# Performance work log

Measured on AMD Instinct MI355X. Metric: run time of the kernel, lower is better.

## Reference

```python
import jax, jax.numpy as jnp
import numpy as np

TIME = 100.0   # self.time in the original module
TAU = 100.0    # decay constant: exp((t - time)/100)


def setup_inputs() -> dict:
    key = jax.random.key(0)
    k1, k2, k3, k4 = jax.random.split(key, 4)
    N, D, B, K = 500000, 128, 50000, 32
    nodes = jax.random.randint(k1, (B,), 0, N)
    neigh_ids = jax.random.randint(k2, (B, K), 0, N)
    # neighbor event times in [0, 200]; only t <= TIME are valid temporal neighbors
    neigh_times = jax.random.uniform(k3, (B, K), dtype=jnp.float32) * 200.0
    features = jax.random.normal(k4, (N, D), dtype=jnp.float32)
    return {"nodes": nodes, "neigh_ids": neigh_ids,
            "neigh_times": neigh_times, "features": features}


def reference(nodes, neigh_ids, neigh_times, features):
    # Time-decayed edge weights; neighbors with t > TIME are masked out
    # (equivalent to the searchsorted cutoff in the original code).
    w = jnp.where(neigh_times <= TIME, jnp.exp((neigh_times - TIME) / TAU), 0.0)  # [B,K]
    total = w.sum(-1)                               # total_value[i]
    total = jnp.where(total == 0.0, 1.0, total)     # fallback to 1 when no valid neighbor
    w = w / total[:, None]                          # dic_edge[i][j] / total_value[i]
    # self-loop weight 1, then row-normalize: num_neigh = 1 + sum_j w_ij
    denom = 1.0 + w.sum(-1)                         # [B]
    neigh_feats = jnp.einsum('bk,bkd->bd', w, features[neigh_ids])  # weighted neighbor sum
    out = (features[nodes] + neigh_feats) / denom[:, None]          # [B,D]
    return out
```

## Files before the change

### kernel.cpp

```cpp
#include <hip/hip_runtime.h>
#include <math.h>


__global__ __launch_bounds__(256) void mean_agg_kernel(
    const int*   __restrict__ nodes,
    const int*   __restrict__ neigh_ids,
    const float* __restrict__ neigh_times,
    const float* __restrict__ features,
    float*       __restrict__ out,
    int B)
{
    const int wave = threadIdx.x >> 6;
    const int lane = threadIdx.x & 63;
    const int row  = blockIdx.x * 4 + wave;
    if (row >= B) return;

    const int j = lane & 31;
    const float t  = neigh_times[row * 32 + j];
    const int  idj = neigh_ids[row * 32 + j];
    float wj = (t <= 100.0f) ? __expf((t - 100.0f) * 0.01f) : 0.0f;

    float S = wj;
    #pragma unroll
    for (int m = 1; m < 32; m <<= 1)
        S += __shfl_xor(S, m);

    const float T     = (S == 0.0f) ? 1.0f : S;
    const float denom = 1.0f + S / T;

    float2 acc = make_float2(0.0f, 0.0f);
    #pragma unroll 4
    for (int k = 0; k < 32; ++k) {
        const float wk = __shfl(wj, k);
        if (wk != 0.0f) {
            const int idk = __shfl(idj, k);
            const float2 f = *reinterpret_cast<const float2*>(
                &features[(size_t)idk * 128 + lane * 2]);
            acc.x += wk * f.x;
            acc.y += wk * f.y;
        }
    }

    const int self = nodes[row];
    const float2 fs = *reinterpret_cast<const float2*>(
        &features[(size_t)self * 128 + lane * 2]);

    const float inv_d  = 1.0f / denom;
    const float inv_td = 1.0f / (T * denom);
    float2 o;
    o.x = fs.x * inv_d + acc.x * inv_td;
    o.y = fs.y * inv_d + acc.y * inv_td;
    *reinterpret_cast<float2*>(&out[(size_t)row * 128 + lane * 2]) = o;
}

extern "C" void kernel_launch(void* const* d_in, const int* in_sizes, int n_in,
                              void* d_out, int out_size, void* d_ws, size_t ws_size,
                              hipStream_t stream) {
    const int*   nodes       = (const int*)  d_in[0];
    const int*   neigh_ids   = (const int*)  d_in[1];
    const float* neigh_times = (const float*)d_in[2];
    const float* features    = (const float*)d_in[3];
    float*       out         = (float*)      d_out;

    const int B = in_sizes[0];
    const int rows_per_block = 4;
    const int grid = (B + rows_per_block - 1) / rows_per_block;

    mean_agg_kernel<<<grid, 256, 0, stream>>>(nodes, neigh_ids, neigh_times,
                                              features, out, B);
}
```

Baseline: 78.60 us.

## Split wave into two half-waves gathering alternate neighbors with float4 loads

Each 64-lane wave now splits into two 32-lane halves. Each half gathers every other neighbor row using 16-byte float4 loads, so two neighbor rows are fetched per iteration, and the two partial sums are combined with a cross-half shuffle. Only the lower half writes the output. The goal is more memory-level parallelism and half as many dependent gather iterations. The cost is extra shuffles, a fully unrolled loop, and redundant self-feature loads in the upper half.

```diff
diff --git a/kernel.cpp b/kernel.cpp
--- a/kernel.cpp
+++ b/kernel.cpp
@@ -12,12 +12,13 @@
 {
     const int wave = threadIdx.x >> 6;
     const int lane = threadIdx.x & 63;
+    const int half = lane >> 5;
+    const int c    = lane & 31;
     const int row  = blockIdx.x * 4 + wave;
     if (row >= B) return;
 
-    const int j = lane & 31;
-    const float t  = neigh_times[row * 32 + j];
-    const int  idj = neigh_ids[row * 32 + j];
+    const float t  = neigh_times[row * 32 + c];
+    const int  idj = neigh_ids[row * 32 + c];
     float wj = (t <= 100.0f) ? __expf((t - 100.0f) * 0.01f) : 0.0f;
 
     float S = wj;
@@ -28,29 +29,40 @@
     const float T     = (S == 0.0f) ? 1.0f : S;
     const float denom = 1.0f + S / T;
 
-    float2 acc = make_float2(0.0f, 0.0f);
-    #pragma unroll 4
-    for (int k = 0; k < 32; ++k) {
-        const float wk = __shfl(wj, k);
+    float4 acc = make_float4(0.0f, 0.0f, 0.0f, 0.0f);
+    #pragma unroll
+    for (int i = 0; i < 16; ++i) {
+        const int   k   = 2 * i + half;
+        const float wk  = __shfl(wj, k);
+        const int   idk = __shfl(idj, k);
         if (wk != 0.0f) {
-            const int idk = __shfl(idj, k);
-            const float2 f = *reinterpret_cast<const float2*>(
-                &features[(size_t)idk * 128 + lane * 2]);
+            const float4 f = *reinterpret_cast<const float4*>(
+                &features[(size_t)idk * 128 + c * 4]);
             acc.x += wk * f.x;
             acc.y += wk * f.y;
+            acc.z += wk * f.z;
+            acc.w += wk * f.w;
         }
     }
+    acc.x += __shfl_xor(acc.x, 32);
+    acc.y += __shfl_xor(acc.y, 32);
+    acc.z += __shfl_xor(acc.z, 32);
+    acc.w += __shfl_xor(acc.w, 32);
 
     const int self = nodes[row];
-    const float2 fs = *reinterpret_cast<const float2*>(
-        &features[(size_t)self * 128 + lane * 2]);
+    const float4 fs = *reinterpret_cast<const float4*>(
+        &features[(size_t)self * 128 + c * 4]);
 
     const float inv_d  = 1.0f / denom;
     const float inv_td = 1.0f / (T * denom);
-    float2 o;
+    float4 o;
     o.x = fs.x * inv_d + acc.x * inv_td;
     o.y = fs.y * inv_d + acc.y * inv_td;
-    *reinterpret_cast<float2*>(&out[(size_t)row * 128 + lane * 2]) = o;
+    o.z = fs.z * inv_d + acc.z * inv_td;
+    o.w = fs.w * inv_d + acc.w * inv_td;
+
+    if (half == 0)
+        *reinterpret_cast<float4*>(&out[(size_t)row * 128 + c * 4]) = o;
 }
 
 extern "C" void kernel_launch(void* const* d_in, const int* in_sizes, int n_in,
```

Measured after the change: 72.41 us. 1.09x faster.

## Split wave into four neighbor groups with 32-byte loads and cross-lane reduction

Applied to the files above, without the earlier changes.

Each wave now processes four neighbors at once. Each 16-lane group gathers one full 512-byte feature row with two 16-byte vector loads per lane, instead of the whole wave loading one row with 8-byte loads per neighbor. Partial sums are combined with xor-shuffles across the groups, and one group writes the output with wide stores. This shortens the serial gather loop from 32 to 8 iterations and raises memory-level parallelism, at the cost of eight extra shuffle rounds and lane divergence on the masked neighbors.

```diff
diff --git a/kernel.cpp b/kernel.cpp
--- a/kernel.cpp
+++ b/kernel.cpp
@@ -1,6 +1,8 @@
 #include <hip/hip_runtime.h>
 #include <math.h>
 
+
+typedef float vfloat4 __attribute__((ext_vector_type(4)));
 
 __global__ __launch_bounds__(256) void mean_agg_kernel(
     const int*   __restrict__ nodes,
@@ -12,6 +14,8 @@
 {
     const int wave = threadIdx.x >> 6;
     const int lane = threadIdx.x & 63;
+    const int q    = lane >> 4;
+    const int c    = lane & 15;
     const int row  = blockIdx.x * 4 + wave;
     if (row >= B) return;
 
@@ -28,29 +32,48 @@
     const float T     = (S == 0.0f) ? 1.0f : S;
     const float denom = 1.0f + S / T;
 
-    float2 acc = make_float2(0.0f, 0.0f);
-    #pragma unroll 4
-    for (int k = 0; k < 32; ++k) {
-        const float wk = __shfl(wj, k);
+    vfloat4 acc0 = (vfloat4)(0.0f);
+    vfloat4 acc1 = (vfloat4)(0.0f);
+    #pragma unroll
+    for (int i = 0; i < 8; ++i) {
+        const int   k   = 4 * i + q;
+        const float wk  = __shfl(wj, k);
+        const int   idk = __shfl(idj, k);
         if (wk != 0.0f) {
-            const int idk = __shfl(idj, k);
-            const float2 f = *reinterpret_cast<const float2*>(
-                &features[(size_t)idk * 128 + lane * 2]);
-            acc.x += wk * f.x;
-            acc.y += wk * f.y;
+            const float* fp = &features[(size_t)idk * 128 + c * 8];
+            const vfloat4 f0 = *reinterpret_cast<const vfloat4*>(fp);
+            const vfloat4 f1 = *reinterpret_cast<const vfloat4*>(fp + 4);
+            acc0 += wk * f0;
+            acc1 += wk * f1;
         }
     }
+    #pragma unroll
+    for (int m = 16; m <= 32; m <<= 1) {
+        acc0.x += __shfl_xor(acc0.x, m);
+        acc0.y += __shfl_xor(acc0.y, m);
+        acc0.z += __shfl_xor(acc0.z, m);
+        acc0.w += __shfl_xor(acc0.w, m);
+        acc1.x += __shfl_xor(acc1.x, m);
+        acc1.y += __shfl_xor(acc1.y, m);
+        acc1.z += __shfl_xor(acc1.z, m);
+        acc1.w += __shfl_xor(acc1.w, m);
+    }
 
-    const int self = nodes[row];
-    const float2 fs = *reinterpret_cast<const float2*>(
-        &features[(size_t)self * 128 + lane * 2]);
+    if (q == 0) {
+        const int self = nodes[row];
+        const float* sp = &features[(size_t)self * 128 + c * 8];
+        const vfloat4 fs0 = *reinterpret_cast<const vfloat4*>(sp);
+        const vfloat4 fs1 = *reinterpret_cast<const vfloat4*>(sp + 4);
 
-    const float inv_d  = 1.0f / denom;
-    const float inv_td = 1.0f / (T * denom);
-    float2 o;
-    o.x = fs.x * inv_d + acc.x * inv_td;
-    o.y = fs.y * inv_d + acc.y * inv_td;
-    *reinterpret_cast<float2*>(&out[(size_t)row * 128 + lane * 2]) = o;
+        const float inv_d  = 1.0f / denom;
+        const float inv_td = 1.0f / (T * denom);
+        const vfloat4 o0 = fs0 * inv_d + acc0 * inv_td;
+        const vfloat4 o1 = fs1 * inv_d + acc1 * inv_td;
+
+        float* op = &out[(size_t)row * 128 + c * 8];
+        *reinterpret_cast<vfloat4*>(op)     = o0;
+        *reinterpret_cast<vfloat4*>(op + 4) = o1;
+    }
 }
 
 extern "C" void kernel_launch(void* const* d_in, const int* in_sizes, int n_in,
```

Result: faster. 71.51 us (-9.0%).
